# Performance work log

Hardware: AMD Instinct MI355X
Metric: run time of the kernel (lower is better)

Reference implementation:

```python
import jax, jax.numpy as jnp
import numpy as np
import math

N_NODES = 100000
N_EDGES = 500000
HEADS = 8
IN_CH = 128          # dim(x) + dim(feats) = 64 + 64
OUT_CH = 128         # heads * 16
HEAD_DIM = OUT_CH // HEADS
MSG_DIM = 64
TIME_DIM = 64
EDGE_DIM = MSG_DIM + TIME_DIM


def setup_inputs() -> dict:
    key = jax.random.key(0)
    ks = jax.random.split(key, 16)
    p = lambda k, shp: (jax.random.normal(k, shp, dtype=jnp.float32) * 0.02)
    return {
        "feats": jax.random.normal(ks[0], (N_NODES, 64), dtype=jnp.float32),
        "x": jax.random.normal(ks[1], (N_NODES, 64), dtype=jnp.float32),
        "last_update": jax.random.uniform(ks[2], (N_NODES,), dtype=jnp.float32),
        "edge_index": jax.random.randint(ks[3], (2, N_EDGES), 0, N_NODES, dtype=jnp.int64),
        "t": jax.random.uniform(ks[4], (N_EDGES,), dtype=jnp.float32),
        "msg": jax.random.normal(ks[5], (N_EDGES, MSG_DIM), dtype=jnp.float32),
        # TimeEncoder: cos(Linear(1, TIME_DIM)(t))
        "time_w": p(ks[6], (TIME_DIM,)),
        "time_b": p(ks[7], (TIME_DIM,)),
        # TransformerConv params
        "Wq": p(ks[8], (IN_CH, OUT_CH)),
        "bq": jnp.zeros((OUT_CH,), jnp.float32),
        "Wk": p(ks[9], (IN_CH, OUT_CH)),
        "bk": jnp.zeros((OUT_CH,), jnp.float32),
        "Wv": p(ks[10], (IN_CH, OUT_CH)),
        "bv": jnp.zeros((OUT_CH,), jnp.float32),
        "We": p(ks[11], (EDGE_DIM, OUT_CH)),   # lin_edge, bias=False in PyG
        "Wskip": p(ks[12], (IN_CH, OUT_CH)),   # root weight skip connection
        "bskip": jnp.zeros((OUT_CH,), jnp.float32),
    }


def reference(feats, x, last_update, edge_index, t, msg,
              time_w, time_b, Wq, bq, Wk, bk, Wv, bv, We, Wskip, bskip):
    N = feats.shape[0]
    src, dst = edge_index[0], edge_index[1]  # message flows src -> dst

    # relative time encoding (TGN time encoder: cos(w*t + b))
    rel_t = last_update[src] - t                                  # [E]
    rel_t_enc = jnp.cos(rel_t[:, None] * time_w[None, :] + time_b)  # [E, TIME_DIM]
    edge_attr = jnp.concatenate([rel_t_enc, msg], axis=-1)        # [E, EDGE_DIM]

    h = jnp.concatenate([x, feats], axis=-1)                      # [N, IN_CH]

    q = (h @ Wq + bq).reshape(N, HEADS, HEAD_DIM)
    k = (h @ Wk + bk).reshape(N, HEADS, HEAD_DIM)
    v = (h @ Wv + bv).reshape(N, HEADS, HEAD_DIM)
    e = (edge_attr @ We).reshape(-1, HEADS, HEAD_DIM)             # [E, H, C]

    k_e = k[src] + e                                              # [E, H, C]
    alpha = jnp.sum(q[dst] * k_e, axis=-1) / math.sqrt(HEAD_DIM)  # [E, H]

    # segment softmax over incoming edges of each dst node
    m = jax.ops.segment_max(alpha, dst, num_segments=N)           # [N, H]
    m = jnp.where(jnp.isfinite(m), m, 0.0)
    ex = jnp.exp(alpha - m[dst])
    s = jax.ops.segment_sum(ex, dst, num_segments=N)              # [N, H]
    a = ex / (s[dst] + 1e-16)                                     # [E, H]

    out_e = (v[src] + e) * a[..., None]                           # [E, H, C]
    out = jax.ops.segment_sum(out_e, dst, num_segments=N)         # [N, H, C]
    out = out.reshape(N, HEADS * HEAD_DIM)
    return out + h @ Wskip + bskip
```

## Files before the change

### kernel.cpp

```cpp
#include <hip/hip_runtime.h>
#include <math.h>


typedef __attribute__((ext_vector_type(8))) short bf16x8;
typedef __attribute__((ext_vector_type(4))) float f32x4;

__device__ inline short f2bf(float f) {
  unsigned u = __float_as_uint(f);
  u += 0x7fff + ((u >> 16) & 1);
  return (short)(u >> 16);
}
__device__ inline float bflo(unsigned u) { return __uint_as_float(u << 16); }
__device__ inline float bfhi(unsigned u) { return __uint_as_float(u & 0xffff0000u); }

struct PrepArgs { const float* W[5]; };
__global__ void k_front(PrepArgs pa, short* __restrict__ wf,
                        const int* __restrict__ ei, int* __restrict__ counts,
                        int E) {
  const int b = blockIdx.x;
  if (b < 40) {
    int tid = b * 256 + threadIdx.x;
    if (tid >= 5 * 8 * 4 * 64) return;
    int lane = tid & 63;
    int kt = (tid >> 6) & 3;
    int nt = (tid >> 8) & 7;
    int mat = tid >> 11;
    const float* W = pa.W[mat];
    int n = nt * 16 + (lane & 15);
    short v[8];
#pragma unroll
    for (int j = 0; j < 8; ++j) {
      int k = kt * 32 + ((j >> 2) * 16) + ((lane >> 4) * 4) + (j & 3);
      v[j] = f2bf(W[k * 128 + n]);
    }
    ((uint4*)wf)[tid] = *(uint4*)v;
  } else {
    int i = (b - 40) * 256 + threadIdx.x;
    if (i < E) atomicAdd(&counts[ei[E + i]], 1);
  }
}

__global__ __launch_bounds__(1024) void k_bsum(const int* __restrict__ counts,
                                               int* __restrict__ bsum, int N) {
  int i = blockIdx.x * 1024 + threadIdx.x;
  int v = (i < N) ? counts[i] : 0;
  for (int d = 32; d; d >>= 1) v += __shfl_down(v, d);
  __shared__ int ws_[16];
  int lane = threadIdx.x & 63, wv = threadIdx.x >> 6;
  if (lane == 0) ws_[wv] = v;
  __syncthreads();
  if (threadIdx.x == 0) {
    int s = 0;
    for (int j = 0; j < 16; ++j) s += ws_[j];
    bsum[blockIdx.x] = s;
  }
}

__global__ __launch_bounds__(1024) void k_scan2(const int* __restrict__ counts,
                                                const int* __restrict__ bsum,
                                                int* __restrict__ offs,
                                                int* __restrict__ cursor,
                                                int N, int nb) {
  __shared__ int sh[1024];
  __shared__ int wsum[16];
  const int t = threadIdx.x;
  const int b = blockIdx.x;
  int pv = (t < b && t < nb) ? bsum[t] : 0;
  for (int d = 32; d; d >>= 1) pv += __shfl_down(pv, d);
  if ((t & 63) == 0) wsum[t >> 6] = pv;
  __syncthreads();
  if (t == 0) {
    int s = 0;
    for (int j = 0; j < 16; ++j) s += wsum[j];
    wsum[0] = s;
  }
  __syncthreads();
  const int bpre = wsum[0];

  int i = b * 1024 + t;
  int v = (i < N) ? counts[i] : 0;
  sh[t] = v;
  __syncthreads();
  for (int d = 1; d < 1024; d <<= 1) {
    int u = (t >= d) ? sh[t - d] : 0;
    __syncthreads();
    sh[t] += u;
    __syncthreads();
  }
  if (i < N) {
    int excl = bpre + sh[t] - v;
    offs[i] = excl;
    cursor[i] = excl;
    if (i == N - 1) offs[N] = excl + v;
  }
}

__global__ void k_scatter(const int* __restrict__ ei, int* __restrict__ cursor,
                          int* __restrict__ rank, int* __restrict__ src_s, int E) {
  int i = blockIdx.x * 256 + threadIdx.x;
  if (i < E) {
    int pos = atomicAdd(&cursor[ei[E + i]], 1);
    rank[i] = pos;
    src_s[pos] = ei[i];
  }
}

struct NodeArgs {
  const short* wf;
  const float* bias[4];
  void* outp[4];
};

__global__ __launch_bounds__(256, 2) void k_node(
    const float* __restrict__ x, const float* __restrict__ feats,
    NodeArgs na, int N) {
  __shared__ char lds[4][8192];
  const int lane = threadIdx.x & 63;
  const int wv = threadIdx.x >> 6;
  char* myl = lds[wv];

  bf16x8 bfrag[8][4];
  const uint4* wfp = (const uint4*)na.wf + (size_t)wv * 2048;
#pragma unroll
  for (int nt = 0; nt < 8; ++nt)
#pragma unroll
    for (int kt = 0; kt < 4; ++kt)
      *(uint4*)&bfrag[nt][kt] = wfp[(nt * 4 + kt) * 64 + lane];

  float biasv[8];
#pragma unroll
  for (int nt = 0; nt < 8; ++nt) biasv[nt] = na.bias[wv][nt * 16 + (lane & 15)];
  void* op = na.outp[wv];

  const int arow = lane & 15;
  const int k4 = (lane >> 4) * 4;
  const int ntiles = (N + 15) / 16;
  for (int tile = blockIdx.x; tile < ntiles; tile += gridDim.x) {
    int row = tile * 16 + arow;
    bool valid = row < N;
    const float* xr = x + (size_t)row * 64;
    const float* fr = feats + (size_t)row * 64;
    bf16x8 afrag[4];
#pragma unroll
    for (int kt = 0; kt < 4; ++kt) {
      const float* src = (kt < 2) ? xr : fr;
      int base = (kt & 1) * 32 + k4;
      float4 lo = valid ? *(const float4*)(src + base) : make_float4(0, 0, 0, 0);
      float4 hi = valid ? *(const float4*)(src + base + 16) : make_float4(0, 0, 0, 0);
      bf16x8 a;
      a[0] = f2bf(lo.x); a[1] = f2bf(lo.y); a[2] = f2bf(lo.z); a[3] = f2bf(lo.w);
      a[4] = f2bf(hi.x); a[5] = f2bf(hi.y); a[6] = f2bf(hi.z); a[7] = f2bf(hi.w);
      afrag[kt] = a;
    }
#pragma unroll
    for (int nt = 0; nt < 8; ++nt) {
      f32x4 acc = {0.f, 0.f, 0.f, 0.f};
#pragma unroll
      for (int kt = 0; kt < 4; ++kt)
        acc = __builtin_amdgcn_mfma_f32_16x16x32_bf16(afrag[kt], bfrag[nt][kt], acc, 0, 0, 0);
      int col = nt * 16 + (lane & 15);
#pragma unroll
      for (int reg = 0; reg < 4; ++reg) {
        int r = (lane >> 4) * 4 + reg;
        float vv = acc[reg] + biasv[nt];
        if (wv < 3) {
          int wb = (r * 256 + col * 2) ^ (((r >> 2) & 3) << 5);
          *(short*)(myl + wb) = f2bf(vv);
        } else {
          int wb = (r * 512 + col * 4) ^ (((r >> 2) & 3) << 6);
          *(float*)(myl + wb) = vv;
        }
      }
    }
    if (wv < 3) {
      short* opp = (short*)op;
#pragma unroll
      for (int i = 0; i < 8; ++i) {
        int r = i * 2 + (lane >> 5);
        int orow = tile * 16 + r;
        int rb = (r * 256 + (lane & 31) * 8) ^ (((r >> 2) & 3) << 5);
        uint2 val = *(const uint2*)(myl + rb);
        if (orow < N)
          *(uint2*)(opp + (size_t)orow * 128 + (lane & 31) * 4) = val;
      }
    } else {
      float* opp = (float*)op;
#pragma unroll
      for (int i = 0; i < 8; ++i) {
        int r = i * 2 + (lane >> 5);
        int orow = tile * 16 + r;
        int rb = (r * 512 + (lane & 31) * 16) ^ (((r >> 2) & 3) << 6);
        uint4 val = *(const uint4*)(myl + rb);
        if (orow < N)
          *(uint4*)(opp + (size_t)orow * 128 + (lane & 31) * 4) = val;
      }
    }
  }
}

__global__ __launch_bounds__(512) void k_egemm(
    const float* __restrict__ lu, const int* __restrict__ ei,
    const float* __restrict__ t, const float* __restrict__ msg,
    const float* __restrict__ tw, const float* __restrict__ tb,
    const short* __restrict__ wf, const int* __restrict__ rank,
    short* __restrict__ e_s, int E) {
  __shared__ uint4 wlds[2048];
  __shared__ char tbuf[8][4096];
  const int lane = threadIdx.x & 63;
  const int wv = threadIdx.x >> 6;
  char* myl = tbuf[wv];

  for (int i = threadIdx.x; i < 2048; i += 512)
    wlds[i] = ((const uint4*)wf)[8192 + i];
  __syncthreads();

  const int k4 = (lane >> 4) * 4;
  float twv[16], tbv[16];
#pragma unroll
  for (int kt = 0; kt < 2; ++kt) {
    int base = kt * 32 + k4;
    *(float4*)&twv[kt * 8]     = *(const float4*)(tw + base);
    *(float4*)&twv[kt * 8 + 4] = *(const float4*)(tw + base + 16);
    *(float4*)&tbv[kt * 8]     = *(const float4*)(tb + base);
    *(float4*)&tbv[kt * 8 + 4] = *(const float4*)(tb + base + 16);
  }

  const int ntiles = (E + 15) / 16;
  const int nwaves = gridDim.x * 8;
  int tile = blockIdx.x * 8 + wv;
  int p_src = 0, p_rank = 0;
  float p_t = 0.f;
  if (tile < ntiles && lane < 16 && tile * 16 + lane < E) {
    p_src  = ei[tile * 16 + lane];
    p_rank = rank[tile * 16 + lane];
    p_t    = t[tile * 16 + lane];
  }
  for (; tile < ntiles; tile += nwaves) {
    const int e0 = tile * 16;
    const int rank16 = p_rank;
    float relt = 0.f;
    if (lane < 16 && e0 + lane < E)
      relt = lu[p_src] - p_t;
    const int ntile = tile + nwaves;
    if (ntile < ntiles && lane < 16 && ntile * 16 + lane < E) {
      p_src  = ei[ntile * 16 + lane];
      p_rank = rank[ntile * 16 + lane];
      p_t    = t[ntile * 16 + lane];
    }
    const int r = lane & 15;
    float my_relt = __shfl(relt, r);
    bool rvalid = (e0 + r) < E;

    bf16x8 afrag[4];
#pragma unroll
    for (int kt = 0; kt < 2; ++kt) {
      bf16x8 a;
#pragma unroll
      for (int j = 0; j < 8; ++j)
        a[j] = f2bf(__cosf(my_relt * twv[kt * 8 + j] + tbv[kt * 8 + j]));
      afrag[kt] = a;
    }
    const float* mr = msg + (size_t)(e0 + r) * 64;
#pragma unroll
    for (int kt = 2; kt < 4; ++kt) {
      int base = (kt - 2) * 32 + k4;
      float4 lo = rvalid ? *(const float4*)(mr + base) : make_float4(0, 0, 0, 0);
      float4 hi = rvalid ? *(const float4*)(mr + base + 16) : make_float4(0, 0, 0, 0);
      bf16x8 a;
      a[0] = f2bf(lo.x); a[1] = f2bf(lo.y); a[2] = f2bf(lo.z); a[3] = f2bf(lo.w);
      a[4] = f2bf(hi.x); a[5] = f2bf(hi.y); a[6] = f2bf(hi.z); a[7] = f2bf(hi.w);
      afrag[kt] = a;
    }

#pragma unroll
    for (int nt = 0; nt < 8; ++nt) {
      bf16x8 bfrag[4];
#pragma unroll
      for (int kt = 0; kt < 4; ++kt)
        *(uint4*)&bfrag[kt] = wlds[(nt * 4 + kt) * 64 + lane];
      f32x4 acc = {0.f, 0.f, 0.f, 0.f};
#pragma unroll
      for (int kt = 0; kt < 4; ++kt)
        acc = __builtin_amdgcn_mfma_f32_16x16x32_bf16(afrag[kt], bfrag[kt], acc, 0, 0, 0);
      int col = nt * 16 + (lane & 15);
#pragma unroll
      for (int reg = 0; reg < 4; ++reg) {
        int rr = (lane >> 4) * 4 + reg;
        int wb = (rr * 256 + col * 2) ^ (((rr >> 2) & 3) << 5);
        *(short*)(myl + wb) = f2bf(acc[reg]);
      }
    }
#pragma unroll
    for (int i = 0; i < 8; ++i) {
      int rr = i * 2 + (lane >> 5);
      int er = e0 + rr;
      int drow = __shfl(rank16, rr);
      int rb = (rr * 256 + (lane & 31) * 8) ^ (((rr >> 2) & 3) << 5);
      uint2 val = *(const uint2*)(myl + rb);
      if (er < E)
        *(uint2*)(e_s + (size_t)drow * 128 + (lane & 31) * 4) = val;
    }
  }
}

__global__ __launch_bounds__(256) void k_agg(
    const int* __restrict__ offs, const int* __restrict__ src_s,
    const short* __restrict__ e_s, const short* __restrict__ qb,
    const short* __restrict__ kb, const short* __restrict__ vb,
    float* __restrict__ out, int N) {
  __shared__ int lds_vo[4][64];
  const int wave = threadIdx.x >> 6;
  const int lane = threadIdx.x & 63;
  const int n0 = (blockIdx.x * 4 + wave) * 2;
  if (n0 >= N) return;
  const int c2 = lane * 2;
  const bool hasB = (n0 + 1) < N;

  const int offA = offs[n0];
  const int endA = offs[n0 + 1];
  const int endB = hasB ? offs[n0 + 2] : endA;
  const int offB = endA;
  unsigned qvA = *(const unsigned*)(qb + (size_t)n0 * 128 + c2);
  unsigned qvB = hasB ? *(const unsigned*)(qb + (size_t)(n0 + 1) * 128 + c2) : 0u;
  float2 oA = *(float2*)(out + (size_t)n0 * 128 + c2);
  float2 oB = hasB ? *(float2*)(out + (size_t)(n0 + 1) * 128 + c2)
                   : make_float2(0.f, 0.f);

  auto process = [&](int off, int end, unsigned qv, float2& o) {
    if (end <= off) return;
    const float q0 = bflo(qv), q1 = bfhi(qv);
    float s = 0.f, acc0 = 0.f, acc1 = 0.f;
    for (int c0 = off; c0 < end; c0 += 64) {
      const int cnt = min(64, end - c0);
      if (lane < cnt) lds_vo[wave][lane] = src_s[c0 + lane] * 128;
      const int lim = cnt - 1;
      for (int g0 = 0; g0 < cnt; g0 += 8) {
        unsigned evr[8], kvr[8], vvr[8];
#pragma unroll
        for (int g = 0; g < 8; ++g) {
          int jj = g0 + g;
          jj = (jj > lim) ? lim : jj;
          int vo = lds_vo[wave][jj];
          evr[g] = *(const unsigned*)(e_s + (size_t)(c0 + jj) * 128 + c2);
          kvr[g] = *(const unsigned*)(kb + vo + c2);
          vvr[g] = *(const unsigned*)(vb + vo + c2);
        }
#pragma unroll
        for (int g = 0; g < 8; ++g) {
          float part = q0 * (bflo(kvr[g]) + bflo(evr[g]))
                     + q1 * (bfhi(kvr[g]) + bfhi(evr[g]));
          part += __shfl_xor(part, 1);
          part += __shfl_xor(part, 2);
          part += __shfl_xor(part, 4);
          float p = (g0 + g <= lim) ? __expf(part * 0.25f) : 0.f;
          s += p;
          acc0 = fmaf(p, bflo(vvr[g]) + bflo(evr[g]), acc0);
          acc1 = fmaf(p, bfhi(vvr[g]) + bfhi(evr[g]), acc1);
        }
      }
    }
    float r = 1.f / (s + 1e-16f);
    o.x += acc0 * r;
    o.y += acc1 * r;
  };

  process(offA, endA, qvA, oA);
  *(float2*)(out + (size_t)n0 * 128 + c2) = oA;
  if (hasB) {
    process(offB, endB, qvB, oB);
    *(float2*)(out + (size_t)(n0 + 1) * 128 + c2) = oB;
  }
}

extern "C" void kernel_launch(void* const* d_in, const int* in_sizes, int n_in,
                              void* d_out, int out_size, void* d_ws, size_t ws_size,
                              hipStream_t stream) {
  const float* feats = (const float*)d_in[0];
  const float* x     = (const float*)d_in[1];
  const float* lu    = (const float*)d_in[2];
  const int*   ei    = (const int*)d_in[3];
  const float* t     = (const float*)d_in[4];
  const float* msg   = (const float*)d_in[5];
  const float* tw    = (const float*)d_in[6];
  const float* tb    = (const float*)d_in[7];
  const float* Wq    = (const float*)d_in[8];
  const float* bq    = (const float*)d_in[9];
  const float* Wk    = (const float*)d_in[10];
  const float* bk    = (const float*)d_in[11];
  const float* Wv    = (const float*)d_in[12];
  const float* bv    = (const float*)d_in[13];
  const float* We    = (const float*)d_in[14];
  const float* Wskip = (const float*)d_in[15];
  const float* bskip = (const float*)d_in[16];
  float* out = (float*)d_out;
  const int N = in_sizes[2];
  const int E = in_sizes[4];

  char* ws = (char*)d_ws;
  short* wfrag = (short*)ws; ws += 5 * 2048 * 16;
  short* qb    = (short*)ws; ws += (size_t)N * 128 * 2;
  short* kbuf  = (short*)ws; ws += (size_t)N * 128 * 2;
  short* vbuf  = (short*)ws; ws += (size_t)N * 128 * 2;
  short* e_s   = (short*)ws; ws += (size_t)E * 128 * 2;
  int* counts  = (int*)ws;   ws += (size_t)(N + 1) * 4;
  int* offs    = (int*)ws;   ws += (size_t)(N + 4) * 4;
  int* cursor  = (int*)ws;   ws += (size_t)N * 4;
  int* rank    = (int*)ws;   ws += (size_t)E * 4;
  int* src_s   = (int*)ws;   ws += (size_t)E * 4;
  int* bsum    = (int*)ws;   ws += 128 * 4;

  const int nb = (N + 1023) / 1024;
  const int nhist = (E + 255) / 256;

  hipMemsetAsync(counts, 0, (size_t)(N + 1) * 4, stream);

  PrepArgs pa;
  pa.W[0] = Wq; pa.W[1] = Wk; pa.W[2] = Wv; pa.W[3] = Wskip; pa.W[4] = We;
  k_front<<<40 + nhist, 256, 0, stream>>>(pa, wfrag, ei, counts, E);

  k_bsum<<<nb, 1024, 0, stream>>>(counts, bsum, N);
  k_scan2<<<nb, 1024, 0, stream>>>(counts, bsum, offs, cursor, N, nb);
  k_scatter<<<nhist, 256, 0, stream>>>(ei, cursor, rank, src_s, E);

  NodeArgs na;
  na.wf = wfrag;
  na.bias[0] = bq; na.bias[1] = bk; na.bias[2] = bv; na.bias[3] = bskip;
  na.outp[0] = qb; na.outp[1] = kbuf; na.outp[2] = vbuf; na.outp[3] = out;
  k_node<<<768, 256, 0, stream>>>(x, feats, na, N);

  k_egemm<<<512, 512, 0, stream>>>(lu, ei, t, msg, tw, tb, wfrag,
                                   rank, e_s, E);
  k_agg<<<(N + 7) / 8, 256, 0, stream>>>(offs, src_s, e_s, qb, kbuf, vbuf,
                                         out, N);
}
```

Before: 275.8 us.

## Fold block-sum into scan and merge scatter into node GEMM launch

Removes the separate k_bsum kernel by having each scan block directly sum all preceding counts, and merges the CSR scatter kernel into the node projection kernel as extra blocks. This cuts two kernel launches and lets the scatter atomics overlap with the node GEMM. In exchange each scan block redundantly reads up to all N counts, a quadratic-ish amount of read work across blocks.

```diff
diff --git a/kernel.cpp b/kernel.cpp
--- a/kernel.cpp
+++ b/kernel.cpp
@@ -40,32 +40,17 @@
   }
 }
 
-__global__ __launch_bounds__(1024) void k_bsum(const int* __restrict__ counts,
-                                               int* __restrict__ bsum, int N) {
-  int i = blockIdx.x * 1024 + threadIdx.x;
-  int v = (i < N) ? counts[i] : 0;
-  for (int d = 32; d; d >>= 1) v += __shfl_down(v, d);
-  __shared__ int ws_[16];
-  int lane = threadIdx.x & 63, wv = threadIdx.x >> 6;
-  if (lane == 0) ws_[wv] = v;
-  __syncthreads();
-  if (threadIdx.x == 0) {
-    int s = 0;
-    for (int j = 0; j < 16; ++j) s += ws_[j];
-    bsum[blockIdx.x] = s;
-  }
-}
-
 __global__ __launch_bounds__(1024) void k_scan2(const int* __restrict__ counts,
-                                                const int* __restrict__ bsum,
                                                 int* __restrict__ offs,
                                                 int* __restrict__ cursor,
-                                                int N, int nb) {
+                                                int N) {
   __shared__ int sh[1024];
   __shared__ int wsum[16];
   const int t = threadIdx.x;
   const int b = blockIdx.x;
-  int pv = (t < b && t < nb) ? bsum[t] : 0;
+  const int base_cnt = b << 10;
+  int pv = 0;
+  for (int i = t; i < base_cnt; i += 1024) pv += counts[i];
   for (int d = 32; d; d >>= 1) pv += __shfl_down(pv, d);
   if ((t & 63) == 0) wsum[t >> 6] = pv;
   __syncthreads();
@@ -77,7 +62,7 @@
   __syncthreads();
   const int bpre = wsum[0];
 
-  int i = b * 1024 + t;
+  int i = base_cnt + t;
   int v = (i < N) ? counts[i] : 0;
   sh[t] = v;
   __syncthreads();
@@ -95,25 +80,25 @@
   }
 }
 
-__global__ void k_scatter(const int* __restrict__ ei, int* __restrict__ cursor,
-                          int* __restrict__ rank, int* __restrict__ src_s, int E) {
-  int i = blockIdx.x * 256 + threadIdx.x;
-  if (i < E) {
-    int pos = atomicAdd(&cursor[ei[E + i]], 1);
-    rank[i] = pos;
-    src_s[pos] = ei[i];
-  }
-}
-
 struct NodeArgs {
   const short* wf;
   const float* bias[4];
   void* outp[4];
 };
 
-__global__ __launch_bounds__(256, 2) void k_node(
+__global__ __launch_bounds__(256, 2) void k_nodescat(
     const float* __restrict__ x, const float* __restrict__ feats,
-    NodeArgs na, int N) {
+    NodeArgs na, int N, const int* __restrict__ ei, int* __restrict__ cursor,
+    int* __restrict__ rank, int* __restrict__ src_s, int E, int nnode) {
+  if (blockIdx.x >= nnode) {
+    int i = (blockIdx.x - nnode) * 256 + threadIdx.x;
+    if (i < E) {
+      int pos = atomicAdd(&cursor[ei[E + i]], 1);
+      rank[i] = pos;
+      src_s[pos] = ei[i];
+    }
+    return;
+  }
   __shared__ char lds[4][8192];
   const int lane = threadIdx.x & 63;
   const int wv = threadIdx.x >> 6;
@@ -135,7 +120,7 @@
   const int arow = lane & 15;
   const int k4 = (lane >> 4) * 4;
   const int ntiles = (N + 15) / 16;
-  for (int tile = blockIdx.x; tile < ntiles; tile += gridDim.x) {
+  for (int tile = blockIdx.x; tile < ntiles; tile += nnode) {
     int row = tile * 16 + arow;
     bool valid = row < N;
     const float* xr = x + (size_t)row * 64;
@@ -407,10 +392,10 @@
   int* cursor  = (int*)ws;   ws += (size_t)N * 4;
   int* rank    = (int*)ws;   ws += (size_t)E * 4;
   int* src_s   = (int*)ws;   ws += (size_t)E * 4;
-  int* bsum    = (int*)ws;   ws += 128 * 4;
 
   const int nb = (N + 1023) / 1024;
   const int nhist = (E + 255) / 256;
+  const int nnode = 768;
 
   hipMemsetAsync(counts, 0, (size_t)(N + 1) * 4, stream);
 
@@ -418,15 +403,14 @@
   pa.W[0] = Wq; pa.W[1] = Wk; pa.W[2] = Wv; pa.W[3] = Wskip; pa.W[4] = We;
   k_front<<<40 + nhist, 256, 0, stream>>>(pa, wfrag, ei, counts, E);
 
-  k_bsum<<<nb, 1024, 0, stream>>>(counts, bsum, N);
-  k_scan2<<<nb, 1024, 0, stream>>>(counts, bsum, offs, cursor, N, nb);
-  k_scatter<<<nhist, 256, 0, stream>>>(ei, cursor, rank, src_s, E);
+  k_scan2<<<nb, 1024, 0, stream>>>(counts, offs, cursor, N);
 
   NodeArgs na;
   na.wf = wfrag;
   na.bias[0] = bq; na.bias[1] = bk; na.bias[2] = bv; na.bias[3] = bskip;
   na.outp[0] = qb; na.outp[1] = kbuf; na.outp[2] = vbuf; na.outp[3] = out;
-  k_node<<<768, 256, 0, stream>>>(x, feats, na, N);
+  k_nodescat<<<nnode + nhist, 256, 0, stream>>>(x, feats, na, N, ei, cursor,
+                                                rank, src_s, E, nnode);
 
   k_egemm<<<512, 512, 0, stream>>>(lu, ei, t, msg, tw, tb, wfrag,
                                    rank, e_s, E);
```

Result: no change. 271.5 us (-1.5%).
